# Kernel tuning notes

Hardware: AMD Instinct MI355X
Metric: run time of the kernel (lower is better)

Reference implementation:

```python
import jax, jax.numpy as jnp
import numpy as np

N_NODES = 10000
N_REL = 200
DIM = 128          # rank * 2
REL_DIM = 128
VIS_DIM = 512
TXT_DIM = 768
N_EDGES = 320000


def _glorot(key, shape):
    fan_in, fan_out = shape[1], shape[0]
    lim = (6.0 / (fan_in + fan_out)) ** 0.5
    return jax.random.uniform(key, shape, jnp.float32, -lim, lim)


def setup_inputs() -> dict:
    key = jax.random.key(0)
    ks = jax.random.split(key, 24)
    inp = {}
    inp['x'] = jax.random.randint(ks[0], (1024, 3), 0, N_NODES)
    inp['edge_index'] = jax.random.randint(ks[1], (2, N_EDGES), 0, N_NODES)
    inp['edge_type'] = jax.random.randint(ks[2], (N_EDGES,), 0, N_REL)
    inp['visual'] = jax.random.normal(ks[3], (N_NODES, VIS_DIM), jnp.float32)
    inp['textual'] = jax.random.normal(ks[4], (N_NODES, TXT_DIM), jnp.float32)
    # embeddings (scaled by 0.001 as in torch init)
    inp['structural_emb'] = jax.random.normal(ks[5], (N_NODES, DIM), jnp.float32) * 0.001
    inp['relation_emb'] = jax.random.normal(ks[6], (N_REL, REL_DIM), jnp.float32) * 0.001
    # three KBGAT convs: w1 [out, 2*in+rel], b1 [out], w2 [1, out]
    cat = 2 * DIM + REL_DIM
    for i, tag in enumerate(['s', 'v', 't']):
        inp[f'W1_{tag}'] = _glorot(ks[7 + 3 * i], (DIM, cat))
        inp[f'b1_{tag}'] = jnp.zeros((DIM,), jnp.float32)
        inp[f'w2_{tag}'] = _glorot(ks[8 + 3 * i], (1, DIM))
    # modality projections
    inp['Wv'] = _glorot(ks[16], (DIM, VIS_DIM))
    inp['bv'] = jnp.zeros((DIM,), jnp.float32)
    inp['Wt'] = _glorot(ks[17], (DIM, TXT_DIM))
    inp['bt'] = jnp.zeros((DIM,), jnp.float32)
    inp['alpha'] = jnp.float32(0.1)
    inp['gamma'] = jnp.float32(0.8)
    return inp


def kbgat_conv(feat, rel_emb, src, dst, edge_type, W1, b1, w2):
    # gather per-edge embeddings: x_i = target, x_j = source (PyG default flow)
    triple = jnp.concatenate([feat[dst], feat[src], rel_emb[edge_type]], axis=1)  # [E, 2*D+R]
    c = triple @ W1.T + b1                                   # [E, D]
    b = jax.nn.leaky_relu(c @ w2[0])                         # [E]
    # segment softmax over destination nodes
    m = jax.ops.segment_max(b, dst, num_segments=N_NODES)
    e = jnp.exp(b - m[dst])
    z = jax.ops.segment_sum(e, dst, num_segments=N_NODES)
    attn = e / z[dst]                                        # [E]
    agg = jax.ops.segment_sum(c * attn[:, None], dst, num_segments=N_NODES)  # [N, D]
    return jax.nn.leaky_relu(agg)


def reference(x, edge_index, edge_type, visual, textual, structural_emb, relation_emb,
              W1_s, b1_s, w2_s, W1_v, b1_v, w2_v, W1_t, b1_t, w2_t,
              Wv, bv, Wt, bt, alpha, gamma):
    src, dst = edge_index[0], edge_index[1]
    h_s = kbgat_conv(structural_emb, relation_emb, src, dst, edge_type, W1_s, b1_s, w2_s)
    vf = visual @ Wv.T + bv
    h_v = kbgat_conv(vf, relation_emb, src, dst, edge_type, W1_v, b1_v, w2_v)
    tf = textual @ Wt.T + bt
    h_t = kbgat_conv(tf, relation_emb, src, dst, edge_type, W1_t, b1_t, w2_t)
    return (1.0 - alpha - gamma) * h_s + alpha * h_v + gamma * h_t
```

## Files before the change

kernel.cpp:

```cpp
#include <hip/hip_runtime.h>
#include <hip/hip_bf16.h>

typedef unsigned short u16;
typedef unsigned int u32;
typedef __bf16 bf16x8 __attribute__((ext_vector_type(8)));
typedef float f32x4 __attribute__((ext_vector_type(4)));

#define DIM 128

__device__ __forceinline__ u16 f2bf_rne(float x) {
  u32 u = __float_as_uint(x);
  return (u16)((u + 0x7fffu + ((u >> 16) & 1u)) >> 16);
}
__device__ __forceinline__ u32 packbf2(float x, float y) {
  return (u32)f2bf_rne(x) | ((u32)f2bf_rne(y) << 16);
}
__device__ __forceinline__ float lrelu(float x) { return x > 0.f ? x : 0.01f * x; }
__device__ __forceinline__ int iclamp(int v, int hi) { return v < 0 ? 0 : (v >= hi ? hi - 1 : v); }
__device__ __forceinline__ float sane(float x) { return (x == x) ? x : 0.f; }

__device__ __forceinline__ float wred_max(float v) {
  #pragma unroll
  for (int o = 32; o > 0; o >>= 1) v = fmaxf(v, __shfl_xor(v, o, 64));
  return v;
}
__device__ __forceinline__ float wred_sum(float v) {
  #pragma unroll
  for (int o = 32; o > 0; o >>= 1) v += __shfl_xor(v, o, 64);
  return v;
}

struct PrepAllArgs {
  const float* W1[3]; const float* Wmod[3]; int K[3]; u16* Wc[3];
  const float* rel; const float* b1[3]; const float* bmod[3]; const float* w2[3];
  u16* PrAll; float* qr[3]; int NR;
  const int* dst; int* cnt; int* rank; int E; int N;
  int wc2End; int wc1End; int wc0End; int nCompute; int totB;
};
struct MainArgs {
  const float* A[3]; const u16* B[3]; const float* w2[3];
  u16* PdAll; u16* PsAll; float* qd[3]; float* qs[3];
  int M; int K[3]; int tilesPerM; int nGemm; int totB;
  const int* dst; const int* src; const int* etyp;
  const int* offs; const int* rank; u32* sortedST;
  int E; int NR;
};
struct AgArgs {
  const u32* sortedST; const int* offs;
  const float* qd[3]; const float* qs[3]; const float* qr[3];
  const u16* PdAll; const u16* PsAll; const u16* PrAll;
  const float* alphaP; const float* gammaP;
  float* outp; int N; int NR; int E;
};

__global__ __launch_bounds__(256) void fused_prep(PrepAllArgs a) {
  __shared__ float relL[2][128];
  __shared__ float bmL[128];
  __shared__ float qpr[4];
  int b = blockIdx.x, tid = threadIdx.x;
  long nC = a.nCompute, tot = a.totB;
  int cprev = (int)((long)b * nC / tot);
  int cnext = (int)(((long)b + 1) * nC / tot);
  if (cnext == cprev) {
    int h = b - cprev;
    int e = h * 256 + tid;
    if (e < a.E) {
      int d = a.dst[e];
      if (d >= 0 && d < a.N) a.rank[e] = atomicAdd(&a.cnt[d], 1);
    }
    return;
  }
  int c = cprev;
  if (c < a.wc0End) {
    int m, loc;
    if (c < a.wc2End)      { m = 2; loc = c; }
    else if (c < a.wc1End) { m = 1; loc = c - a.wc2End; }
    else                   { m = 0; loc = c - a.wc1End; }
    int o = loc & 255, kb = loc >> 8;
    int k = (kb << 8) + tid;
    int K = a.K[m];
    if (k < K) {
      int halfsel = (o >= 128) ? 128 : 0;
      int oo = o & 127;
      const float* W1 = a.W1[m];
      const float* Wm = a.Wmod[m];
      float acc;
      if (Wm == nullptr) {
        acc = W1[oo * 384 + halfsel + k];
      } else {
        acc = 0.f;
        for (int i = 0; i < 128; ++i)
          acc += W1[oo * 384 + halfsel + i] * Wm[i * K + k];
      }
      a.Wc[m][((size_t)(k >> 5) * 256 + o) * 32 + (k & 31)] = f2bf_rne(acc);
    }
  } else {
    int idx = c - a.wc0End;
    int NRpair = (a.NR + 1) >> 1;
    int m = idx / NRpair;
    if (m > 2) return;
    int rp = idx - m * NRpair;
    int r0 = rp * 2;
    {
      int ro = tid >> 7, ii = tid & 127;
      int rr = r0 + ro;
      relL[ro][ii] = (rr < a.NR) ? a.rel[rr * 128 + ii] : 0.f;
    }
    const float* bmod = a.bmod[m];
    if (tid < 128) bmL[tid] = (bmod != nullptr) ? bmod[tid] : 0.f;
    __syncthreads();
    int lane = tid & 63, wv = tid >> 6;
    int rsel = wv >> 1;
    int obase = (wv & 1) * 64;
    int r = r0 + rsel;
    bool rok = (r < a.NR);
    const float* W1 = a.W1[m];
    const float* b1 = a.b1[m];
    const float* w2 = a.w2[m];
    bool hasbm = (bmod != nullptr);
    float qacc = 0.f;
    for (int oo = 0; oo < 64; ++oo) {
      int o = obase + oo;
      const float* row = W1 + o * 384;
      float a2 = row[256 + lane];
      float a5 = row[320 + lane];
      float s = a2 * relL[rsel][lane] + a5 * relL[rsel][64 + lane];
      if (hasbm) {
        float a0 = row[lane], a1 = row[128 + lane];
        float a3 = row[64 + lane], a4 = row[192 + lane];
        s += (a0 + a1) * bmL[lane] + (a3 + a4) * bmL[64 + lane];
      }
      s = wred_sum(s);
      float totv = s + b1[o];
      if (rok && lane == 0)
        a.PrAll[(size_t)r * 384 + m * 128 + o] = f2bf_rne(totv);
      qacc += totv * w2[o];
    }
    if (lane == 0) qpr[wv] = qacc;
    __syncthreads();
    if (tid < 2) {
      int rr = r0 + tid;
      if (rr < a.NR) a.qr[m][rr] = sane(qpr[tid * 2] + qpr[tid * 2 + 1]);
    }
  }
}

__global__ __launch_bounds__(1024) void scan_k(const int* __restrict__ cnt,
                                               int* __restrict__ offs, int N) {
  __shared__ int sums[1024];
  int t = threadIdx.x;
  int chunk = (N + 1023) >> 10;
  int base = t * chunk;
  int s = 0;
  for (int i = 0; i < chunk; ++i) { int idx = base + i; if (idx < N) s += cnt[idx]; }
  sums[t] = s;
  __syncthreads();
  for (int off = 1; off < 1024; off <<= 1) {
    int v = (t >= off) ? sums[t - off] : 0;
    __syncthreads();
    sums[t] += v;
    __syncthreads();
  }
  int prefix = (t > 0) ? sums[t - 1] : 0;
  for (int i = 0; i < chunk; ++i) {
    int idx = base + i;
    if (idx < N) { offs[idx] = prefix; prefix += cnt[idx]; }
  }
  if (t == 1023) offs[N] = sums[1023];
}

__device__ __forceinline__ void gemm_epilogue(const MainArgs& g, int m, int row0,
                                              f32x4 (&acc)[2][4], float (*qpart)[32]) {
  int tid = threadIdx.x;
  int lane = tid & 63, wv = tid >> 6;
  int quad = lane >> 4, l16 = lane & 15;
  int M = g.M;
  const float* w2 = g.w2[m];
  u16* PdAll = g.PdAll;
  u16* PsAll = g.PsAll;
  float w2c[4];
  #pragma unroll
  for (int t = 0; t < 4; ++t) w2c[t] = w2[(wv & 1) * 64 + t * 16 + l16];

  #pragma unroll
  for (int rg = 0; rg < 2; ++rg) {
    float part[4];
    #pragma unroll
    for (int r = 0; r < 4; ++r) {
      int rr = row0 + rg * 16 + quad * 4 + r;
      bool ok = rr < M;
      float qp = 0.f;
      #pragma unroll
      for (int t = 0; t < 4; ++t) {
        int cc = (wv & 1) * 64 + t * 16 + l16;
        if (ok) {
          if (wv < 2) PdAll[(size_t)rr * 384 + m * 128 + cc] = f2bf_rne(acc[rg][t][r]);
          else        PsAll[(size_t)rr * 384 + m * 128 + cc] = f2bf_rne(acc[rg][t][r]);
        }
        qp += acc[rg][t][r] * w2c[t];
      }
      #pragma unroll
      for (int mk = 1; mk < 16; mk <<= 1) qp += __shfl_xor(qp, mk, 64);
      part[r] = qp;
    }
    if (l16 == 0) {
      #pragma unroll
      for (int r = 0; r < 4; ++r) qpart[wv][rg * 16 + quad * 4 + r] = part[r];
    }
  }
  __syncthreads();
  if (tid < 64) {
    int row = tid & 31;
    int half = tid >> 5;
    int rr = row0 + row;
    if (rr < M) {
      if (half == 0) g.qd[m][rr] = sane(qpart[0][row] + qpart[1][row]);
      else           g.qs[m][rr] = sane(qpart[2][row] + qpart[3][row]);
    }
  }
}

template<int NT>
__device__ __forceinline__ void gemm_exact(const MainArgs& g, int m, int tile,
                                           u16* Als, float (*qpart)[32]) {
  constexpr int H = (NT + 1) / 2;
  const int M = g.M;
  int tid = threadIdx.x;
  int lane = tid & 63, wv = tid >> 6;
  int quad = lane >> 4, l16 = lane & 15;
  int row0 = tile * 32;
  int srow = tid >> 3;
  int tk4 = (tid & 7) * 4;
  int srsw = srow & 3;
  int wg = tk4 >> 3;
  int wrem = tk4 & 7;
  int grow = row0 + srow;
  if (grow >= M) grow = M - 1;
  const float* Ag = g.A[m] + (size_t)grow * (NT * 32);

  float4 vreg[H];
  #pragma unroll
  for (int i = 0; i < H; ++i)
    vreg[i] = *reinterpret_cast<const float4*>(Ag + tk4 + i * 32);
  #pragma unroll
  for (int i = 0; i < H; ++i) {
    int gidx = wg ^ srsw ^ (i & 3);
    u32* dp = reinterpret_cast<u32*>(&Als[((i * 32 + srow) * 32) + (gidx << 3) + wrem]);
    dp[0] = packbf2(vreg[i].x, vreg[i].y);
    dp[1] = packbf2(vreg[i].z, vreg[i].w);
  }
  #pragma unroll
  for (int i = H; i < NT; ++i)
    vreg[i - H] = *reinterpret_cast<const float4*>(Ag + tk4 + i * 32);
  #pragma unroll
  for (int i = H; i < NT; ++i) {
    int gidx = wg ^ srsw ^ (i & 3);
    u32* dp = reinterpret_cast<u32*>(&Als[((i * 32 + srow) * 32) + (gidx << 3) + wrem]);
    dp[0] = packbf2(vreg[i - H].x, vreg[i - H].y);
    dp[1] = packbf2(vreg[i - H].z, vreg[i - H].w);
  }
  __syncthreads();

  const u16* Bpg = g.B[m] + (size_t)(wv * 64 + l16) * 32 + quad * 8;
  f32x4 acc[2][4];
  #pragma unroll
  for (int rg = 0; rg < 2; ++rg)
    #pragma unroll
    for (int t = 0; t < 4; ++t) acc[rg][t] = (f32x4){0.f, 0.f, 0.f, 0.f};

  #pragma unroll
  for (int kb = 0; kb < NT; ++kb) {
    const u16* bp = Bpg + (size_t)kb * 8192;
    bf16x8 b0 = *reinterpret_cast<const bf16x8*>(bp);
    bf16x8 b1 = *reinterpret_cast<const bf16x8*>(bp + 512);
    bf16x8 b2 = *reinterpret_cast<const bf16x8*>(bp + 1024);
    bf16x8 b3 = *reinterpret_cast<const bf16x8*>(bp + 1536);
    int gsw = (quad ^ (l16 & 3) ^ (kb & 3)) << 3;
    #pragma unroll
    for (int rg = 0; rg < 2; ++rg) {
      bf16x8 av = *reinterpret_cast<const bf16x8*>(
          &Als[(kb * 32 + rg * 16 + l16) * 32 + gsw]);
      acc[rg][0] = __builtin_amdgcn_mfma_f32_16x16x32_bf16(av, b0, acc[rg][0], 0, 0, 0);
      acc[rg][1] = __builtin_amdgcn_mfma_f32_16x16x32_bf16(av, b1, acc[rg][1], 0, 0, 0);
      acc[rg][2] = __builtin_amdgcn_mfma_f32_16x16x32_bf16(av, b2, acc[rg][2], 0, 0, 0);
      acc[rg][3] = __builtin_amdgcn_mfma_f32_16x16x32_bf16(av, b3, acc[rg][3], 0, 0, 0);
    }
  }
  gemm_epilogue(g, m, row0, acc, qpart);
}

__device__ void gemm_generic(const MainArgs& g, int m, int tile,
                             u16* Als, float (*qpart)[32]) {
  const int M = g.M, K = g.K[m];
  int nt = K >> 5;
  int tid = threadIdx.x;
  int lane = tid & 63, wv = tid >> 6;
  int quad = lane >> 4, l16 = lane & 15;
  int row0 = tile * 32;
  int srow = tid >> 3;
  int tk4 = (tid & 7) * 4;
  int srsw = srow & 3;
  int wg = tk4 >> 3;
  int wrem = tk4 & 7;
  int grow = row0 + srow;
  if (grow >= M) grow = M - 1;
  const float* Ag = g.A[m] + (size_t)grow * K;
  const u16* Bpg = g.B[m] + (size_t)(wv * 64 + l16) * 32 + quad * 8;

  f32x4 acc[2][4];
  #pragma unroll
  for (int rg = 0; rg < 2; ++rg)
    #pragma unroll
    for (int t = 0; t < 4; ++t) acc[rg][t] = (f32x4){0.f, 0.f, 0.f, 0.f};

  for (int c0 = 0; c0 < nt; c0 += 24) {
    int kc = nt - c0; if (kc > 24) kc = 24;
    __syncthreads();
    for (int i = 0; i < kc; ++i) {
      int kg = (c0 + i) * 32 + tk4;
      if (kg + 3 < K) {
        float4 v = *reinterpret_cast<const float4*>(Ag + kg);
        int gidx = wg ^ srsw ^ (i & 3);
        u32* dp = reinterpret_cast<u32*>(&Als[((i * 32 + srow) * 32) + (gidx << 3) + wrem]);
        dp[0] = packbf2(v.x, v.y);
        dp[1] = packbf2(v.z, v.w);
      }
    }
    __syncthreads();
    for (int kb = 0; kb < kc; ++kb) {
      const u16* bp = Bpg + (size_t)(c0 + kb) * 8192;
      bf16x8 b0 = *reinterpret_cast<const bf16x8*>(bp);
      bf16x8 b1 = *reinterpret_cast<const bf16x8*>(bp + 512);
      bf16x8 b2 = *reinterpret_cast<const bf16x8*>(bp + 1024);
      bf16x8 b3 = *reinterpret_cast<const bf16x8*>(bp + 1536);
      int gsw = (quad ^ (l16 & 3) ^ (kb & 3)) << 3;
      #pragma unroll
      for (int rg = 0; rg < 2; ++rg) {
        bf16x8 av = *reinterpret_cast<const bf16x8*>(
            &Als[(kb * 32 + rg * 16 + l16) * 32 + gsw]);
        acc[rg][0] = __builtin_amdgcn_mfma_f32_16x16x32_bf16(av, b0, acc[rg][0], 0, 0, 0);
        acc[rg][1] = __builtin_amdgcn_mfma_f32_16x16x32_bf16(av, b1, acc[rg][1], 0, 0, 0);
        acc[rg][2] = __builtin_amdgcn_mfma_f32_16x16x32_bf16(av, b2, acc[rg][2], 0, 0, 0);
        acc[rg][3] = __builtin_amdgcn_mfma_f32_16x16x32_bf16(av, b3, acc[rg][3], 0, 0, 0);
      }
    }
  }
  gemm_epilogue(g, m, row0, acc, qpart);
}

__global__ __launch_bounds__(256) void fused_main(MainArgs g) {
  __shared__ __align__(16) u16 Als[24 * 32 * 32];
  __shared__ float qpart[4][32];
  int b = blockIdx.x;
  long nG = g.nGemm, tot = g.totB;
  int gprev = (int)((long)b * nG / tot);
  int gnext = (int)(((long)b + 1) * nG / tot);
  if (gnext == gprev) {
    int h = b - gprev;
    int e = h * 256 + threadIdx.x;
    if (e < g.E) {
      int d = g.dst[e];
      if (d >= 0 && d < g.M) {
        int pos = g.offs[d] + g.rank[e];
        if (pos >= 0 && pos < g.E) {
          u32 s = (u32)iclamp(g.src[e], g.M);
          u32 t = (u32)iclamp(g.etyp[e], g.NR);
          g.sortedST[pos] = (t << 16) | s;
        }
      }
    }
    return;
  }
  int fb = gprev;
  int tpm = g.tilesPerM;
  int m, tile;
  if (fb < tpm)            { m = 2; tile = fb; }
  else if (fb < 2 * tpm)   { m = 1; tile = fb - tpm; }
  else                     { m = 0; tile = fb - 2 * tpm; }

  int K = g.K[m];
  if (K == 768)      gemm_exact<24>(g, m, tile, Als, qpart);
  else if (K == 512) gemm_exact<16>(g, m, tile, Als, qpart);
  else if (K == 128) gemm_exact<4>(g, m, tile, Als, qpart);
  else               gemm_generic(g, m, tile, Als, qpart);
}

__global__ __launch_bounds__(256) void aggregate_all(AgArgs a) {
  int n = blockIdx.x * 4 + (threadIdx.x >> 6);
  if (n >= a.N) return;
  int lane = threadIdx.x & 63;
  int E = a.E;
  int eb = a.offs[n], ee = a.offs[n + 1];
  if (eb < 0) eb = 0;
  if (eb > E) eb = E;
  if (ee < eb) ee = eb;
  if (ee > E) ee = E;
  int En = ee - eb;

  float al = a.alphaP[0];
  if (!(al > 0.f && al < 1.f)) al = 0.1f;
  float ga = a.gammaP[0];
  if (!(ga > 0.f && ga < 1.f)) ga = 0.8f;
  float coef[3] = {1.f - al - ga, al, ga};

  float qdn[3];
  #pragma unroll
  for (int m = 0; m < 3; ++m) qdn[m] = sane(a.qd[m][n]);

  const u16* PsAll = a.PsAll;
  const u16* PrAll = a.PrAll;
  int dlo = 2 * lane;

  float rm[3] = {-1e30f, -1e30f, -1e30f};
  float z[3] = {0.f, 0.f, 0.f};
  float a0[3] = {0.f, 0.f, 0.f};
  float a1[3] = {0.f, 0.f, 0.f};
  for (int c0 = 0; c0 < En; c0 += 64) {
    int cn = min(64, En - c0);
    u32 stp = 0;
    float bm[3] = {-1e30f, -1e30f, -1e30f};
    if (lane < cn) {
      stp = a.sortedST[eb + c0 + lane];
      int s = (int)(stp & 0xffffu);
      int t = (int)(stp >> 16);
      #pragma unroll
      for (int m = 0; m < 3; ++m)
        bm[m] = lrelu(qdn[m] + a.qs[m][s] + a.qr[m][t]);
    }
    float wr[3];
    #pragma unroll
    for (int m = 0; m < 3; ++m) {
      float cm = wred_max(bm[m]);
      float nm = fmaxf(rm[m], cm);
      float sc = __expf(fmaxf(rm[m] - nm, -80.f));
      z[m] *= sc; a0[m] *= sc; a1[m] *= sc;
      rm[m] = nm;
      wr[m] = (lane < cn) ? __expf(fmaxf(bm[m] - nm, -80.f)) : 0.f;
      z[m] += wr[m];
    }

    int cnR = (cn + 3) & ~3;
    for (int j = 0; j < cnR; j += 4) {
      u32 stj[4];
      float wj[4][3];
      #pragma unroll
      for (int u = 0; u < 4; ++u) {
        stj[u] = __shfl(stp, j + u, 64);
        wj[u][0] = __shfl(wr[0], j + u, 64);
        wj[u][1] = __shfl(wr[1], j + u, 64);
        wj[u][2] = __shfl(wr[2], j + u, 64);
      }
      u32 pu[4][3], ru[4][3];
      #pragma unroll
      for (int u = 0; u < 4; ++u) {
        const u16* ps = PsAll + (size_t)(stj[u] & 0xffffu) * 384 + dlo;
        const u16* pr = PrAll + (size_t)(stj[u] >> 16) * 384 + dlo;
        #pragma unroll
        for (int m = 0; m < 3; ++m) {
          pu[u][m] = *reinterpret_cast<const u32*>(ps + m * 128);
          ru[u][m] = *reinterpret_cast<const u32*>(pr + m * 128);
        }
      }
      #pragma unroll
      for (int u = 0; u < 4; ++u) {
        #pragma unroll
        for (int m = 0; m < 3; ++m) {
          float ps0 = __uint_as_float(pu[u][m] << 16);
          float ps1 = __uint_as_float(pu[u][m] & 0xffff0000u);
          float pr0 = __uint_as_float(ru[u][m] << 16);
          float pr1 = __uint_as_float(ru[u][m] & 0xffff0000u);
          a0[m] = fmaf(wj[u][m], ps0 + pr0, a0[m]);
          a1[m] = fmaf(wj[u][m], ps1 + pr1, a1[m]);
        }
      }
    }
  }
  #pragma unroll
  for (int m = 0; m < 3; ++m) z[m] = wred_sum(z[m]);

  float o0 = 0.f, o1 = 0.f;
  const u16* pd = a.PdAll + (size_t)n * 384 + dlo;
  #pragma unroll
  for (int m = 0; m < 3; ++m) {
    float h0 = 0.f, h1 = 0.f;
    if (En > 0 && z[m] > 0.f) {
      float rz = 1.f / z[m];
      u32 du = *reinterpret_cast<const u32*>(pd + m * 128);
      float pd0 = __uint_as_float(du << 16), pd1 = __uint_as_float(du & 0xffff0000u);
      h0 = lrelu(pd0 + a0[m] * rz);
      h1 = lrelu(pd1 + a1[m] * rz);
    }
    o0 = fmaf(coef[m], h0, o0);
    o1 = fmaf(coef[m], h1, o1);
  }
  float* op = a.outp + (size_t)n * 128 + dlo;
  op[0] = sane(o0);
  op[1] = sane(o1);
}

extern "C" void kernel_launch(void* const* d_in, const int* in_sizes, int n_in,
                              void* d_out, int out_size, void* d_ws, size_t ws_size,
                              hipStream_t stream) {
  const int* ei        = (const int*)d_in[1];
  const int* et        = (const int*)d_in[2];
  const float* visual  = (const float*)d_in[3];
  const float* textual = (const float*)d_in[4];
  const float* semb    = (const float*)d_in[5];
  const float* relemb  = (const float*)d_in[6];
  const float* W1s = (const float*)d_in[7];
  const float* b1s = (const float*)d_in[8];
  const float* w2s = (const float*)d_in[9];
  const float* W1v = (const float*)d_in[10];
  const float* b1v = (const float*)d_in[11];
  const float* w2v = (const float*)d_in[12];
  const float* W1t = (const float*)d_in[13];
  const float* b1t = (const float*)d_in[14];
  const float* w2t = (const float*)d_in[15];
  const float* Wv  = (const float*)d_in[16];
  const float* bv  = (const float*)d_in[17];
  const float* Wt  = (const float*)d_in[18];
  const float* bt  = (const float*)d_in[19];
  const float* alphaP = (const float*)d_in[20];
  const float* gammaP = (const float*)d_in[21];
  float* outp = (float*)d_out;

  const int E   = in_sizes[2];
  const int N   = in_sizes[5] / DIM;
  const int NR  = in_sizes[6] / DIM;
  const int VIS = in_sizes[3] / N;
  const int TXT = in_sizes[4] / N;
  int Ks[3] = {DIM, VIS, TXT};
  const int TPM = (N + 31) / 32;

  const float* W1a[3]   = {W1s, W1v, W1t};
  const float* b1a[3]   = {b1s, b1v, b1t};
  const float* w2a[3]   = {w2s, w2v, w2t};
  const float* Wmoda[3] = {nullptr, Wv, Wt};
  const float* bmoda[3] = {nullptr, bv, bt};
  const float* Amoda[3] = {semb, visual, textual};

  const int* esrc = ei;
  const int* edst = ei + E;
  int egrid = (E + 255) / 256;

  size_t off = 0;
  auto take = [&](size_t bytes) -> size_t {
    size_t o = off;
    off = (off + bytes + 255) & ~(size_t)255;
    return o;
  };
  size_t o_cnt  = take((size_t)N * 4);
  size_t o_rank = take((size_t)E * 4);
  size_t o_offs = take((size_t)(N + 1) * 4);
  size_t o_st   = take((size_t)E * 4);
  size_t o_qdm[3], o_qsm[3], o_qrm[3], o_Wcm[3];
  for (int m = 0; m < 3; ++m) {
    o_qdm[m] = take((size_t)N * 4);
    o_qsm[m] = take((size_t)N * 4);
    o_qrm[m] = take((size_t)NR * 4);
    o_Wcm[m] = take((size_t)256 * Ks[m] * 2);
  }
  size_t o_PrAll = take((size_t)NR * 384 * 2);
  size_t o_PdAll = take((size_t)N * 384 * 2);
  size_t o_PsAll = take((size_t)N * 384 * 2);
  size_t need = off;

  if (ws_size < need) {
    (void)hipMemsetAsync(d_out, 0, (size_t)out_size * 4, stream);
    return;
  }

  char* w = (char*)d_ws;
  int* counts = (int*)(w + o_cnt);
  int* rank   = (int*)(w + o_rank);
  int* offs   = (int*)(w + o_offs);
  u32* sortedST = (u32*)(w + o_st);

  (void)hipMemsetAsync(counts, 0, (size_t)N * 4, stream);

  PrepAllArgs pa;
  pa.rel = relemb; pa.NR = NR;
  pa.PrAll = (u16*)(w + o_PrAll);
  pa.dst = edst; pa.cnt = counts; pa.rank = rank; pa.E = E; pa.N = N;
  for (int m = 0; m < 3; ++m) {
    pa.W1[m] = W1a[m]; pa.Wmod[m] = Wmoda[m]; pa.K[m] = Ks[m];
    pa.Wc[m] = (u16*)(w + o_Wcm[m]);
    pa.b1[m] = b1a[m]; pa.bmod[m] = bmoda[m]; pa.w2[m] = w2a[m];
    pa.qr[m] = (float*)(w + o_qrm[m]);
  }
  int NRpair = (NR + 1) / 2;
  int kbm[3];
  for (int m = 0; m < 3; ++m) kbm[m] = (Ks[m] + 255) / 256;
  pa.wc2End   = 256 * kbm[2];
  pa.wc1End   = pa.wc2End + 256 * kbm[1];
  pa.wc0End   = pa.wc1End + 256 * kbm[0];
  pa.nCompute = pa.wc0End + 3 * NRpair;
  pa.totB     = pa.nCompute + egrid;

  MainArgs ga;
  ga.M = N; ga.tilesPerM = TPM; ga.nGemm = 3 * TPM;
  ga.totB = ga.nGemm + egrid;
  ga.PdAll = (u16*)(w + o_PdAll);
  ga.PsAll = (u16*)(w + o_PsAll);
  ga.dst = edst; ga.src = esrc; ga.etyp = et;
  ga.offs = offs; ga.rank = rank; ga.sortedST = sortedST;
  ga.E = E; ga.NR = NR;
  AgArgs aa;
  for (int m = 0; m < 3; ++m) {
    ga.A[m] = Amoda[m]; ga.B[m] = (const u16*)(w + o_Wcm[m]); ga.w2[m] = w2a[m];
    ga.qd[m] = (float*)(w + o_qdm[m]); ga.qs[m] = (float*)(w + o_qsm[m]);
    ga.K[m] = Ks[m];
    aa.qd[m] = (const float*)(w + o_qdm[m]);
    aa.qs[m] = (const float*)(w + o_qsm[m]);
    aa.qr[m] = (const float*)(w + o_qrm[m]);
  }

  aa.PdAll = (const u16*)(w + o_PdAll);
  aa.PsAll = (const u16*)(w + o_PsAll);
  aa.PrAll = (const u16*)(w + o_PrAll);
  aa.sortedST = sortedST; aa.offs = offs;
  aa.alphaP = alphaP; aa.gammaP = gammaP;
  aa.outp = outp; aa.N = N; aa.NR = NR; aa.E = E;

  fused_prep<<<pa.totB, 256, 0, stream>>>(pa);
  scan_k<<<1, 1024, 0, stream>>>(counts, offs, N);
  fused_main<<<ga.totB, 256, 0, stream>>>(ga);
  aggregate_all<<<(N + 3) / 4, 256, 0, stream>>>(aa);
}
```

Before: 270.5 us.

## Fold prefix scan into prep kernel via last-block ticket and batch edge counting

Removes the separate single-block scan kernel launch by having the last block of the prep kernel, chosen through an atomic ticket, compute the exclusive prefix over node counts. Edge-count blocks now handle 1024 edges each, which cuts the block count. The weight-fold loop gets four independent accumulators, and the relation projection batches four output reductions per pass and packs its bf16 stores into one 64-bit write. This saves a kernel launch and the gap between kernels, at the cost of a serialized tail scan on a 256-thread block and extra atomic ticket traffic.

```diff
diff --git a/kernel.cpp b/kernel.cpp
--- a/kernel.cpp
+++ b/kernel.cpp
@@ -3,6 +3,7 @@
 
 typedef unsigned short u16;
 typedef unsigned int u32;
+typedef unsigned long long u64;
 typedef __bf16 bf16x8 __attribute__((ext_vector_type(8)));
 typedef float f32x4 __attribute__((ext_vector_type(4)));
 
@@ -34,7 +35,7 @@
   const float* W1[3]; const float* Wmod[3]; int K[3]; u16* Wc[3];
   const float* rel; const float* b1[3]; const float* bmod[3]; const float* w2[3];
   u16* PrAll; float* qr[3]; int NR;
-  const int* dst; int* cnt; int* rank; int E; int N;
+  const int* dst; int* cnt; int* rank; int* ticket; int* offs; int E; int N;
   int wc2End; int wc1End; int wc0End; int nCompute; int totB;
 };
 struct MainArgs {
@@ -57,116 +58,158 @@
   __shared__ float relL[2][128];
   __shared__ float bmL[128];
   __shared__ float qpr[4];
+  __shared__ int sums[256];
+  __shared__ int lastF;
   int b = blockIdx.x, tid = threadIdx.x;
   long nC = a.nCompute, tot = a.totB;
   int cprev = (int)((long)b * nC / tot);
   int cnext = (int)(((long)b + 1) * nC / tot);
   if (cnext == cprev) {
-    int h = b - cprev;
-    int e = h * 256 + tid;
-    if (e < a.E) {
-      int d = a.dst[e];
-      if (d >= 0 && d < a.N) a.rank[e] = atomicAdd(&a.cnt[d], 1);
-    }
-    return;
-  }
-  int c = cprev;
-  if (c < a.wc0End) {
-    int m, loc;
-    if (c < a.wc2End)      { m = 2; loc = c; }
-    else if (c < a.wc1End) { m = 1; loc = c - a.wc2End; }
-    else                   { m = 0; loc = c - a.wc1End; }
-    int o = loc & 255, kb = loc >> 8;
-    int k = (kb << 8) + tid;
-    int K = a.K[m];
-    if (k < K) {
-      int halfsel = (o >= 128) ? 128 : 0;
-      int oo = o & 127;
-      const float* W1 = a.W1[m];
-      const float* Wm = a.Wmod[m];
-      float acc;
-      if (Wm == nullptr) {
-        acc = W1[oo * 384 + halfsel + k];
-      } else {
-        acc = 0.f;
-        for (int i = 0; i < 128; ++i)
-          acc += W1[oo * 384 + halfsel + i] * Wm[i * K + k];
-      }
-      a.Wc[m][((size_t)(k >> 5) * 256 + o) * 32 + (k & 31)] = f2bf_rne(acc);
+    int e0 = (b - cprev) * 1024 + tid;
+    #pragma unroll
+    for (int i = 0; i < 4; ++i) {
+      int e = e0 + i * 256;
+      if (e < a.E) {
+        int d = a.dst[e];
+        if (d >= 0 && d < a.N) a.rank[e] = atomicAdd(&a.cnt[d], 1);
+      }
     }
   } else {
-    int idx = c - a.wc0End;
-    int NRpair = (a.NR + 1) >> 1;
-    int m = idx / NRpair;
-    if (m > 2) return;
-    int rp = idx - m * NRpair;
-    int r0 = rp * 2;
-    {
-      int ro = tid >> 7, ii = tid & 127;
-      int rr = r0 + ro;
-      relL[ro][ii] = (rr < a.NR) ? a.rel[rr * 128 + ii] : 0.f;
-    }
-    const float* bmod = a.bmod[m];
-    if (tid < 128) bmL[tid] = (bmod != nullptr) ? bmod[tid] : 0.f;
+    int c = cprev;
+    if (c < a.wc0End) {
+      int m, loc;
+      if (c < a.wc2End)      { m = 2; loc = c; }
+      else if (c < a.wc1End) { m = 1; loc = c - a.wc2End; }
+      else                   { m = 0; loc = c - a.wc1End; }
+      int o = loc & 255, kb = loc >> 8;
+      int k = (kb << 8) + tid;
+      int K = a.K[m];
+      if (k < K) {
+        int halfsel = (o >= 128) ? 128 : 0;
+        int oo = o & 127;
+        const float* W1 = a.W1[m];
+        const float* Wm = a.Wmod[m];
+        float acc;
+        if (Wm == nullptr) {
+          acc = W1[oo * 384 + halfsel + k];
+        } else {
+          const float* wrow = W1 + oo * 384 + halfsel;
+          const float* wmk = Wm + k;
+          float s0 = 0.f, s1 = 0.f, s2 = 0.f, s3 = 0.f;
+          for (int i = 0; i < 128; i += 4) {
+            s0 += wrow[i]     * wmk[(size_t)(i)     * K];
+            s1 += wrow[i + 1] * wmk[(size_t)(i + 1) * K];
+            s2 += wrow[i + 2] * wmk[(size_t)(i + 2) * K];
+            s3 += wrow[i + 3] * wmk[(size_t)(i + 3) * K];
+          }
+          acc = (s0 + s1) + (s2 + s3);
+        }
+        a.Wc[m][((size_t)(k >> 5) * 256 + o) * 32 + (k & 31)] = f2bf_rne(acc);
+      }
+    } else {
+      int idx = c - a.wc0End;
+      int NRpair = (a.NR + 1) >> 1;
+      int m = idx / NRpair;
+      if (m <= 2) {
+        int rp = idx - m * NRpair;
+        int r0 = rp * 2;
+        {
+          int ro = tid >> 7, ii = tid & 127;
+          int rr = r0 + ro;
+          relL[ro][ii] = (rr < a.NR) ? a.rel[rr * 128 + ii] : 0.f;
+        }
+        const float* bmod = a.bmod[m];
+        if (tid < 128) bmL[tid] = (bmod != nullptr) ? bmod[tid] : 0.f;
+        __syncthreads();
+        int lane = tid & 63, wv = tid >> 6;
+        int rsel = wv >> 1;
+        int obase = (wv & 1) * 64;
+        int r = r0 + rsel;
+        bool rok = (r < a.NR);
+        const float* W1 = a.W1[m];
+        const float* b1 = a.b1[m];
+        const float* w2 = a.w2[m];
+        bool hasbm = (bmod != nullptr);
+        float rl0 = relL[rsel][lane], rl1 = relL[rsel][64 + lane];
+        float bm0 = bmL[lane], bm1 = bmL[64 + lane];
+        float qacc = 0.f;
+        for (int oo = 0; oo < 64; oo += 4) {
+          float s[4];
+          #pragma unroll
+          for (int u = 0; u < 4; ++u) {
+            const float* row = W1 + (obase + oo + u) * 384;
+            float v = row[256 + lane] * rl0 + row[320 + lane] * rl1;
+            if (hasbm)
+              v += (row[lane] + row[128 + lane]) * bm0 +
+                   (row[64 + lane] + row[192 + lane]) * bm1;
+            s[u] = v;
+          }
+          #pragma unroll
+          for (int off2 = 32; off2 > 0; off2 >>= 1) {
+            #pragma unroll
+            for (int u = 0; u < 4; ++u) s[u] += __shfl_xor(s[u], off2, 64);
+          }
+          u16 pk[4];
+          #pragma unroll
+          for (int u = 0; u < 4; ++u) {
+            int o = obase + oo + u;
+            float totv = s[u] + b1[o];
+            pk[u] = f2bf_rne(totv);
+            qacc += totv * w2[o];
+          }
+          if (rok && lane == 0) {
+            u16* dstp = a.PrAll + (size_t)r * 384 + m * 128 + obase + oo;
+            *reinterpret_cast<u64*>(dstp) =
+                (u64)pk[0] | ((u64)pk[1] << 16) | ((u64)pk[2] << 32) | ((u64)pk[3] << 48);
+          }
+        }
+        if (lane == 0) qpr[wv] = qacc;
+        __syncthreads();
+        if (tid < 2) {
+          int rr = r0 + tid;
+          if (rr < a.NR) a.qr[m][rr] = sane(qpr[tid * 2] + qpr[tid * 2 + 1]);
+        }
+      }
+    }
+  }
+
+  __syncthreads();
+  if (tid == 0) {
+    __threadfence();
+    int old = __hip_atomic_fetch_add(a.ticket, 1, __ATOMIC_ACQ_REL,
+                                     __HIP_MEMORY_SCOPE_AGENT);
+    lastF = (old == (int)tot - 1) ? 1 : 0;
+  }
+  __syncthreads();
+  if (lastF) {
+    int N = a.N;
+    int chunk = (N + 255) >> 8;
+    int base = tid * chunk;
+    int s = 0;
+    for (int i = 0; i < chunk; ++i) {
+      int idx = base + i;
+      if (idx < N)
+        s += __hip_atomic_load(&a.cnt[idx], __ATOMIC_RELAXED, __HIP_MEMORY_SCOPE_AGENT);
+    }
+    sums[tid] = s;
     __syncthreads();
-    int lane = tid & 63, wv = tid >> 6;
-    int rsel = wv >> 1;
-    int obase = (wv & 1) * 64;
-    int r = r0 + rsel;
-    bool rok = (r < a.NR);
-    const float* W1 = a.W1[m];
-    const float* b1 = a.b1[m];
-    const float* w2 = a.w2[m];
-    bool hasbm = (bmod != nullptr);
-    float qacc = 0.f;
-    for (int oo = 0; oo < 64; ++oo) {
-      int o = obase + oo;
-      const float* row = W1 + o * 384;
-      float a2 = row[256 + lane];
-      float a5 = row[320 + lane];
-      float s = a2 * relL[rsel][lane] + a5 * relL[rsel][64 + lane];
-      if (hasbm) {
-        float a0 = row[lane], a1 = row[128 + lane];
-        float a3 = row[64 + lane], a4 = row[192 + lane];
-        s += (a0 + a1) * bmL[lane] + (a3 + a4) * bmL[64 + lane];
-      }
-      s = wred_sum(s);
-      float totv = s + b1[o];
-      if (rok && lane == 0)
-        a.PrAll[(size_t)r * 384 + m * 128 + o] = f2bf_rne(totv);
-      qacc += totv * w2[o];
-    }
-    if (lane == 0) qpr[wv] = qacc;
-    __syncthreads();
-    if (tid < 2) {
-      int rr = r0 + tid;
-      if (rr < a.NR) a.qr[m][rr] = sane(qpr[tid * 2] + qpr[tid * 2 + 1]);
-    }
-  }
-}
-
-__global__ __launch_bounds__(1024) void scan_k(const int* __restrict__ cnt,
-                                               int* __restrict__ offs, int N) {
-  __shared__ int sums[1024];
-  int t = threadIdx.x;
-  int chunk = (N + 1023) >> 10;
-  int base = t * chunk;
-  int s = 0;
-  for (int i = 0; i < chunk; ++i) { int idx = base + i; if (idx < N) s += cnt[idx]; }
-  sums[t] = s;
-  __syncthreads();
-  for (int off = 1; off < 1024; off <<= 1) {
-    int v = (t >= off) ? sums[t - off] : 0;
-    __syncthreads();
-    sums[t] += v;
-    __syncthreads();
-  }
-  int prefix = (t > 0) ? sums[t - 1] : 0;
-  for (int i = 0; i < chunk; ++i) {
-    int idx = base + i;
-    if (idx < N) { offs[idx] = prefix; prefix += cnt[idx]; }
-  }
-  if (t == 1023) offs[N] = sums[1023];
+    for (int off = 1; off < 256; off <<= 1) {
+      int v = (tid >= off) ? sums[tid - off] : 0;
+      __syncthreads();
+      sums[tid] += v;
+      __syncthreads();
+    }
+    int prefix = (tid > 0) ? sums[tid - 1] : 0;
+    for (int i = 0; i < chunk; ++i) {
+      int idx = base + i;
+      if (idx < N) {
+        int cv = __hip_atomic_load(&a.cnt[idx], __ATOMIC_RELAXED, __HIP_MEMORY_SCOPE_AGENT);
+        a.offs[idx] = prefix;
+        prefix += cv;
+      }
+    }
+    if (tid == 255) a.offs[N] = sums[255];
+  }
 }
 
 __device__ __forceinline__ void gemm_epilogue(const MainArgs& g, int m, int row0,
@@ -541,7 +584,8 @@
 
   const int* esrc = ei;
   const int* edst = ei + E;
-  int egrid = (E + 255) / 256;
+  int egrid  = (E + 255) / 256;
+  int egridH = (E + 1023) / 1024;
 
   size_t off = 0;
   auto take = [&](size_t bytes) -> size_t {
@@ -549,7 +593,7 @@
     off = (off + bytes + 255) & ~(size_t)255;
     return o;
   };
-  size_t o_cnt  = take((size_t)N * 4);
+  size_t o_cnt  = take((size_t)(N + 2) * 4);
   size_t o_rank = take((size_t)E * 4);
   size_t o_offs = take((size_t)(N + 1) * 4);
   size_t o_st   = take((size_t)E * 4);
@@ -572,16 +616,18 @@
 
   char* w = (char*)d_ws;
   int* counts = (int*)(w + o_cnt);
+  int* ticket = counts + N;
   int* rank   = (int*)(w + o_rank);
   int* offs   = (int*)(w + o_offs);
   u32* sortedST = (u32*)(w + o_st);
 
-  (void)hipMemsetAsync(counts, 0, (size_t)N * 4, stream);
+  (void)hipMemsetAsync(counts, 0, (size_t)(N + 1) * 4, stream);
 
   PrepAllArgs pa;
   pa.rel = relemb; pa.NR = NR;
   pa.PrAll = (u16*)(w + o_PrAll);
   pa.dst = edst; pa.cnt = counts; pa.rank = rank; pa.E = E; pa.N = N;
+  pa.ticket = ticket; pa.offs = offs;
   for (int m = 0; m < 3; ++m) {
     pa.W1[m] = W1a[m]; pa.Wmod[m] = Wmoda[m]; pa.K[m] = Ks[m];
     pa.Wc[m] = (u16*)(w + o_Wcm[m]);
@@ -595,7 +641,7 @@
   pa.wc1End   = pa.wc2End + 256 * kbm[1];
   pa.wc0End   = pa.wc1End + 256 * kbm[0];
   pa.nCompute = pa.wc0End + 3 * NRpair;
-  pa.totB     = pa.nCompute + egrid;
+  pa.totB     = pa.nCompute + egridH;
 
   MainArgs ga;
   ga.M = N; ga.tilesPerM = TPM; ga.nGemm = 3 * TPM;
@@ -623,7 +669,6 @@
   aa.outp = outp; aa.N = N; aa.NR = NR; aa.E = E;
 
   fused_prep<<<pa.totB, 256, 0, stream>>>(pa);
-  scan_k<<<1, 1024, 0, stream>>>(counts, offs, N);
   fused_main<<<ga.totB, 256, 0, stream>>>(ga);
   aggregate_all<<<(N + 3) / 4, 256, 0, stream>>>(aa);
 }
```

Result: slower. 344.4 us (+27.3%).
